# Kernel optimization log

Measured on AMD Instinct MI355X. Metric: run time of the kernel, lower is better.

Reference implementation:

```python
import jax, jax.numpy as jnp
import numpy as np

S, B, D, H = 1024, 8, 768, 12
PROMPT_NUM = 8
DH = D // H


def setup_inputs() -> dict:
    key = jax.random.key(0)
    ks = jax.random.split(key, 5)
    scale = 1.0 / np.sqrt(D)
    return {
        "x": jax.random.normal(ks[0], (S, B, D), dtype=jnp.float32),
        "in_proj_weight": jax.random.normal(ks[1], (3 * D, D), dtype=jnp.float32) * scale,
        "in_proj_bias": jax.random.normal(ks[2], (3 * D,), dtype=jnp.float32) * 0.02,
        "out_w": jax.random.normal(ks[3], (D, D), dtype=jnp.float32) * scale,
        "out_b": jax.random.normal(ks[4], (D,), dtype=jnp.float32) * 0.02,
    }


def reference(x, in_proj_weight, in_proj_bias, out_w, out_b):
    # x: (S, B, D) -> (B, S, D)
    xt = jnp.transpose(x, (1, 0, 2))
    qkv = xt @ in_proj_weight.T + in_proj_bias  # (B, S, 3D)
    q, k, v = jnp.split(qkv, 3, axis=-1)
    q = q.reshape(B, S, H, DH)
    k = k.reshape(B, S, H, DH)
    v = v.reshape(B, S, H, DH)
    # affinity (n, q, k, h); scale by sqrt(head_dim)
    aff = jnp.einsum("nqhc,nkhc->nqkh", q / np.sqrt(DH), k)
    # prompt masking: CLS_MASK | PROMPT_MASK
    tokens = S - PROMPT_NUM
    m = np.zeros((S, S), dtype=bool)
    m[0, tokens:] = True          # CLS_MASK: CLS query can't attend to prompts
    m[tokens:, tokens:] = True    # PROMPT_MASK: prompts can't attend to prompts
    m = jnp.asarray(m)
    aff = jnp.where(m[None, :, :, None], jnp.float32(-10000.0), aff)
    # softmax over key axis (dim=-2 of nqkh)
    aff = jax.nn.softmax(aff, axis=2)
    mix = jnp.einsum("nqlh,nlhc->nqhc", aff, v)  # (B, S, H, DH)
    out = mix.reshape(B, S, D) @ out_w.T + out_b
    # transpose back to (S, B, ...)
    return (
        jnp.transpose(q, (1, 0, 2, 3)),
        jnp.transpose(k, (1, 0, 2, 3)),
        jnp.transpose(v, (1, 0, 2, 3)),
        jnp.transpose(out, (1, 0, 2)),
    )
```

## Files before the change

kernel.cpp:

```cpp
#include <hip/hip_runtime.h>
#include <hip/hip_bf16.h>


typedef unsigned short u16;
typedef __attribute__((ext_vector_type(8))) short short8;
typedef __attribute__((ext_vector_type(4))) short short4v;
typedef __attribute__((ext_vector_type(4))) float floatx4;
typedef __attribute__((ext_vector_type(4))) unsigned short ushort4v;
typedef __attribute__((ext_vector_type(2))) unsigned int uint2v;

#define NB 8
#define NS 1024
#define NH 12
#define ND 768
#define DHD 64
#define TOKENS 1016
#define QKV_OUT_STRIDE 6291456

#if __has_builtin(__builtin_amdgcn_exp2f)
#define EXP2(x) __builtin_amdgcn_exp2f(x)
#else
#define EXP2(x) exp2f(x)
#endif

#if defined(__HIP_DEVICE_COMPILE__)
  #if __has_builtin(__builtin_amdgcn_mfma_f32_16x16x16bf16_1k)
    #define MFMA16(a, b, c) __builtin_amdgcn_mfma_f32_16x16x16bf16_1k(a, b, c, 0, 0, 0)
  #else
    #define MFMA16(a, b, c) __builtin_amdgcn_mfma_f32_16x16x16_bf16(a, b, c, 0, 0, 0)
  #endif
  #define GLD16(g, l)                                                        \
    __builtin_amdgcn_global_load_lds(                                        \
        (const __attribute__((address_space(1))) void*)(g),                  \
        (__attribute__((address_space(3))) void*)(l), 16, 0, 0)
#else
  #define MFMA16(a, b, c) (c)
  #define GLD16(g, l) ((void)0)
#endif

__device__ __forceinline__ u16 f2bf(float f) {
  union { float f; unsigned u; } c; c.f = f;
  return (u16)((c.u + 0x7fffu + ((c.u >> 16) & 1u)) >> 16);
}

#define CVT_B0 6144
#define CVT_B1 1728
#define CVT_B2 576
__global__ __launch_bounds__(256) void cvt3(
    const float* __restrict__ s0, u16* __restrict__ d0,
    const float* __restrict__ s1, u16* __restrict__ d1,
    const float* __restrict__ s2, u16* __restrict__ d2) {
  int blk = blockIdx.x;
  if (blk < CVT_B0) {
    const int i = (blk * 256 + (int)threadIdx.x) * 4;
    const float4 v = *(const float4*)(s0 + i);
    const int sb = i / ND;
    const int dd = i - sb * ND;
    const int m = ((sb & 7) << 10) | (sb >> 3);
    ushort4v o;
    o.x = f2bf(v.x); o.y = f2bf(v.y); o.z = f2bf(v.z); o.w = f2bf(v.w);
    *(ushort4v*)(d0 + m * ND + dd) = o;
    return;
  }
  const float* s; u16* d;
  if (blk < CVT_B0 + CVT_B1) { s = s1; d = d1; blk -= CVT_B0; }
  else { s = s2; d = d2; blk -= CVT_B0 + CVT_B1; }
  const int i = (blk * 256 + (int)threadIdx.x) * 4;
  const float4 v = *(const float4*)(s + i);
  ushort4v o;
  o.x = f2bf(v.x); o.y = f2bf(v.y); o.z = f2bf(v.z); o.w = f2bf(v.w);
  *(ushort4v*)(d + i) = o;
}

#define GEMM_STAGE(buf, k0)                                                  \
  do {                                                                       \
    GLD16(ga0 + (k0), &buf##A[c0 * 16][0]);                                  \
    GLD16(ga1 + (k0), &buf##A[c0 * 16 + 16][0]);                             \
    GLD16(gb0 + (k0), &buf##B[c0 * 16][0]);                                  \
    GLD16(gb1 + (k0), &buf##B[c0 * 16 + 16][0]);                             \
  } while (0)

#define GEMM_COMPUTE(buf)                                                    \
  do {                                                                       \
    short8 af[4], bfr[4];                                                    \
    _Pragma("unroll")                                                        \
    for (int mt = 0; mt < 4; ++mt)                                           \
      af[mt] = *(const short8*)&buf##A[wm * 64 + mt * 16 + l15][quad * 8];   \
    _Pragma("unroll")                                                        \
    for (int nt = 0; nt < 4; ++nt)                                           \
      bfr[nt] = *(const short8*)&buf##B[wn * 64 + nt * 16 + l15][quad * 8];  \
    _Pragma("unroll")                                                        \
    for (int mt = 0; mt < 4; ++mt)                                           \
      _Pragma("unroll")                                                      \
      for (int nt = 0; nt < 4; ++nt)                                         \
        acc[mt][nt] = __builtin_amdgcn_mfma_f32_16x16x32_bf16(               \
            af[mt], bfr[nt], acc[mt][nt], 0, 0, 0);                          \
  } while (0)

__global__ __launch_bounds__(256) void qkv_gemm(
    const u16* __restrict__ Xb, const u16* __restrict__ Wb,
    const float* __restrict__ bias, float* __restrict__ out) {
  __shared__ __align__(16) u16 p0A[128][32];
  __shared__ __align__(16) u16 p0B[128][32];
  __shared__ __align__(16) u16 p1A[128][32];
  __shared__ __align__(16) u16 p1B[128][32];
  const int tid = threadIdx.x;
  const int lane = tid & 63, wave = tid >> 6;
  const int l15 = lane & 15, quad = lane >> 4;
  const int wm = wave & 1, wn = wave >> 1;
  const int L = (int)blockIdx.x + 64 * (int)blockIdx.y;
  const int xcd = L & 7, i = L >> 3;
  const int mblk = (xcd + 8 * (i & 7)) * 128;
  const int nblk = (i >> 3) * 128;

  floatx4 acc[4][4];
#pragma unroll
  for (int i2 = 0; i2 < 4; ++i2)
#pragma unroll
    for (int j = 0; j < 4; ++j) acc[i2][j] = (floatx4)0.f;

  const int lr = lane >> 2;
  const int lc = (lane & 3) * 8;
  const int c0 = wave * 2;
  const int r0 = c0 * 16 + lr, r1 = r0 + 16;
  const u16* ga0 = Xb + (mblk + r0) * ND + lc;
  const u16* ga1 = Xb + (mblk + r1) * ND + lc;
  const u16* gb0 = Wb + (nblk + r0) * ND + lc;
  const u16* gb1 = Wb + (nblk + r1) * ND + lc;

  GEMM_STAGE(p0, 0);
  __syncthreads();
  for (int kt = 0; kt < 24; kt += 2) {
    GEMM_STAGE(p1, (kt + 1) * 32);
    GEMM_COMPUTE(p0);
    __syncthreads();
    if (kt + 2 < 24) GEMM_STAGE(p0, (kt + 2) * 32);
    GEMM_COMPUTE(p1);
    __syncthreads();
  }

  const int seg = nblk / ND;
  const int nbase = nblk - seg * ND;
  float* outp = out + seg * QKV_OUT_STRIDE;
#pragma unroll
  for (int mt = 0; mt < 4; ++mt) {
#pragma unroll
    for (int r = 0; r < 4; ++r) {
      const int gm = mblk + wm * 64 + mt * 16 + quad * 4 + r;
      const int b = gm >> 10, s = gm & 1023;
#pragma unroll
      for (int nt = 0; nt < 4; ++nt) {
        const int gn = nblk + wn * 64 + nt * 16 + l15;
        const int nn = nbase + wn * 64 + nt * 16 + l15;
        outp[(s * NB + b) * ND + nn] = acc[mt][nt][r] + bias[gn];
      }
    }
  }
}

__global__ __launch_bounds__(256) void prep(
    const float* __restrict__ K, const float* __restrict__ V,
    u16* __restrict__ Kb, u16* __restrict__ Vt) {
  __shared__ u16 tile[DHD][40];
  const int t = threadIdx.x;
  const int bh = blockIdx.y;
  const int b = bh / NH, h = bh % NH;
  const int s0 = blockIdx.x * 32;
  const int sl = t >> 3;
  const int c0 = (t & 7) * 8;
  const int s = s0 + sl;
  if (blockIdx.z == 0) {
    const float* src = K + ((s * NB + b) * NH + h) * DHD + c0;
    const float4 v0 = *(const float4*)src;
    const float4 v1 = *(const float4*)(src + 4);
    short8 o;
    o[0] = f2bf(v0.x); o[1] = f2bf(v0.y); o[2] = f2bf(v0.z); o[3] = f2bf(v0.w);
    o[4] = f2bf(v1.x); o[5] = f2bf(v1.y); o[6] = f2bf(v1.z); o[7] = f2bf(v1.w);
    *(short8*)(Kb + ((size_t)bh * NS + s) * DHD + c0) = o;
  } else {
    const float* src = V + ((s * NB + b) * NH + h) * DHD + c0;
    const float4 v0 = *(const float4*)src;
    const float4 v1 = *(const float4*)(src + 4);
    tile[c0 + 0][sl] = f2bf(v0.x); tile[c0 + 1][sl] = f2bf(v0.y);
    tile[c0 + 2][sl] = f2bf(v0.z); tile[c0 + 3][sl] = f2bf(v0.w);
    tile[c0 + 4][sl] = f2bf(v1.x); tile[c0 + 5][sl] = f2bf(v1.y);
    tile[c0 + 6][sl] = f2bf(v1.z); tile[c0 + 7][sl] = f2bf(v1.w);
    __syncthreads();
    const int c = t >> 2;
    const int so = (t & 3) * 8;
    *(short8*)(Vt + ((size_t)bh * DHD + c) * NS + s0 + so) =
        *(const short8*)&tile[c][so];
  }
}

__global__ __launch_bounds__(256) void attn(
    const float* __restrict__ Q, const u16* __restrict__ Kb,
    const u16* __restrict__ Vt, u16* __restrict__ mix) {
  __shared__ __align__(16) u16 Kt[64][72];
  __shared__ __align__(16) u16 Vs[64][72];
  const int tid = threadIdx.x;
  const int lane = tid & 63, wave = tid >> 6;
  const int l15 = lane & 15, quad = lane >> 4;
  const int L = (int)blockIdx.x + 8 * (int)blockIdx.y;
  const int xcd = L & 7, tt = L >> 3;
  const int bh = xcd + 8 * (tt >> 3);
  const int qx = tt & 7;
  const int b = bh / NH, h = bh % NH;
  const int qb = qx * 128 + wave * 32;

  const float SC = 0.125f * 1.44269504089f;

  short8 qf[2][2];
  bool qmask[2];
#pragma unroll
  for (int j = 0; j < 2; ++j) {
    const int qj = qb + j * 16 + l15;
    qmask[j] = (qj == 0 || qj >= TOKENS);
    const float* qp = Q + ((qj * NB + b) * NH + h) * DHD + quad * 8;
#pragma unroll
    for (int e = 0; e < 8; ++e) {
      qf[j][0][e] = (short)f2bf(qp[e] * SC);
      qf[j][1][e] = (short)f2bf(qp[32 + e] * SC);
    }
  }

  floatx4 O[2][4];
#pragma unroll
  for (int j = 0; j < 2; ++j)
#pragma unroll
    for (int g = 0; g < 4; ++g) O[j][g] = (floatx4)0.f;
  floatx4 liacc[2];
  liacc[0] = (floatx4)0.f;
  liacc[1] = (floatx4)0.f;
  short4v ones4;
#pragma unroll
  for (int e = 0; e < 4; ++e) ones4[e] = (short)0x3F80;

  const u16* kg = Kb + (size_t)bh * NS * DHD;
  const u16* vg = Vt + (size_t)bh * DHD * NS;

  const int srow = tid >> 2;
  const int scol = (tid & 3) * 16;

  short8 pk0, pk1, pv0, pv1;
  {
    pk0 = *(const short8*)(kg + srow * DHD + scol);
    pk1 = *(const short8*)(kg + srow * DHD + scol + 8);
    pv0 = *(const short8*)(vg + srow * NS + scol);
    pv1 = *(const short8*)(vg + srow * NS + scol + 8);
  }

  for (int it = 0; it < 16; ++it) {
    *(short8*)&Kt[srow][scol] = pk0;
    *(short8*)&Kt[srow][scol + 8] = pk1;
    *(short8*)&Vs[srow][scol] = pv0;
    *(short8*)&Vs[srow][scol + 8] = pv1;
    __syncthreads();
    if (it < 15) {
      const int k0 = (it + 1) * 64;
      pk0 = *(const short8*)(kg + (k0 + srow) * DHD + scol);
      pk1 = *(const short8*)(kg + (k0 + srow) * DHD + scol + 8);
      pv0 = *(const short8*)(vg + srow * NS + k0 + scol);
      pv1 = *(const short8*)(vg + srow * NS + k0 + scol + 8);
    }
    const bool mrow = (it == 15) && (quad >= 2);
#pragma unroll
    for (int sub = 0; sub < 4; ++sub) {
      const short8 kf0 = *(const short8*)&Kt[sub * 16 + l15][quad * 8];
      const short8 kf1 = *(const short8*)&Kt[sub * 16 + l15][32 + quad * 8];
      short4v pb[2];
#pragma unroll
      for (int j = 0; j < 2; ++j) {
        floatx4 a = (floatx4)0.f;
        a = __builtin_amdgcn_mfma_f32_16x16x32_bf16(kf0, qf[j][0], a, 0, 0, 0);
        a = __builtin_amdgcn_mfma_f32_16x16x32_bf16(kf1, qf[j][1], a, 0, 0, 0);
        float p[4];
#pragma unroll
        for (int r = 0; r < 4; ++r) p[r] = EXP2(a[r]);
        if (sub == 3 && mrow && qmask[j]) {
#pragma unroll
          for (int r = 0; r < 4; ++r) p[r] = 0.f;
        }
        __hip_bfloat162 w0 = __float22bfloat162_rn(make_float2(p[0], p[1]));
        __hip_bfloat162 w1 = __float22bfloat162_rn(make_float2(p[2], p[3]));
        uint2v pw;
        pw.x = *(const unsigned*)&w0;
        pw.y = *(const unsigned*)&w1;
        pb[j] = __builtin_bit_cast(short4v, pw);
      }
#pragma unroll
      for (int g = 0; g < 4; ++g) {
        const short4v vf = *(const short4v*)&Vs[g * 16 + l15][sub * 16 + quad * 4];
        O[0][g] = MFMA16(vf, pb[0], O[0][g]);
        O[1][g] = MFMA16(vf, pb[1], O[1][g]);
      }
      liacc[0] = MFMA16(ones4, pb[0], liacc[0]);
      liacc[1] = MFMA16(ones4, pb[1], liacc[1]);
    }
    __syncthreads();
  }

#pragma unroll
  for (int j = 0; j < 2; ++j) {
    const float rl = 1.0f / liacc[j][0];
    const int qj = qb + j * 16 + l15;
    u16* mp = mix + ((size_t)b * NS + qj) * ND + h * DHD + quad * 4;
#pragma unroll
    for (int g = 0; g < 4; ++g) {
      ushort4v o;
#pragma unroll
      for (int r = 0; r < 4; ++r) o[r] = f2bf(O[j][g][r] * rl);
      *(ushort4v*)(mp + g * 16) = o;
    }
  }
}

__global__ __launch_bounds__(256) void out_gemm(
    const u16* __restrict__ A, const u16* __restrict__ Wb,
    const float* __restrict__ bias, float* __restrict__ out) {
  __shared__ __align__(16) u16 p0A[128][32];
  __shared__ __align__(16) u16 p0B[128][32];
  __shared__ __align__(16) u16 p1A[128][32];
  __shared__ __align__(16) u16 p1B[128][32];
  const int tid = threadIdx.x;
  const int lane = tid & 63, wave = tid >> 6;
  const int l15 = lane & 15, quad = lane >> 4;
  const int wm = wave & 1, wn = wave >> 1;
  const int L = (int)blockIdx.x + 64 * (int)blockIdx.y;
  const int xcd = L & 7, i = L >> 3;
  const int mblk = (xcd + 8 * (i & 7)) * 128;
  const int nblk = (i >> 3) * 128;

  floatx4 acc[4][4];
#pragma unroll
  for (int i2 = 0; i2 < 4; ++i2)
#pragma unroll
    for (int j = 0; j < 4; ++j) acc[i2][j] = (floatx4)0.f;

  const int lr = lane >> 2;
  const int lc = (lane & 3) * 8;
  const int c0 = wave * 2;
  const int r0 = c0 * 16 + lr, r1 = r0 + 16;
  const u16* ga0 = A + (mblk + r0) * ND + lc;
  const u16* ga1 = A + (mblk + r1) * ND + lc;
  const u16* gb0 = Wb + (nblk + r0) * ND + lc;
  const u16* gb1 = Wb + (nblk + r1) * ND + lc;

  GEMM_STAGE(p0, 0);
  __syncthreads();
  for (int kt = 0; kt < 24; kt += 2) {
    GEMM_STAGE(p1, (kt + 1) * 32);
    GEMM_COMPUTE(p0);
    __syncthreads();
    if (kt + 2 < 24) GEMM_STAGE(p0, (kt + 2) * 32);
    GEMM_COMPUTE(p1);
    __syncthreads();
  }

#pragma unroll
  for (int mt = 0; mt < 4; ++mt) {
#pragma unroll
    for (int r = 0; r < 4; ++r) {
      const int gm = mblk + wm * 64 + mt * 16 + quad * 4 + r;
      const int b = gm >> 10, s = gm & 1023;
#pragma unroll
      for (int nt = 0; nt < 4; ++nt) {
        const int gn = nblk + wn * 64 + nt * 16 + l15;
        out[(s * NB + b) * ND + gn] = acc[mt][nt][r] + bias[gn];
      }
    }
  }
}

extern "C" void kernel_launch(void* const* d_in, const int* in_sizes, int n_in,
                              void* d_out, int out_size, void* d_ws, size_t ws_size,
                              hipStream_t stream) {
  const float* X  = (const float*)d_in[0];
  const float* W  = (const float*)d_in[1];
  const float* Bi = (const float*)d_in[2];
  const float* Ow = (const float*)d_in[3];
  const float* Ob = (const float*)d_in[4];
  float* out = (float*)d_out;

  u16* Xb  = (u16*)d_ws;
  u16* Wb  = Xb  + 6291456;
  u16* Owb = Wb  + 1769472;
  u16* Vt  = Owb + 589824;
  u16* Kb  = Vt  + 6291456;
  u16* mix = Kb  + 6291456;

  cvt3<<<CVT_B0 + CVT_B1 + CVT_B2, 256, 0, stream>>>(X, Xb, W, Wb, Ow, Owb);
  qkv_gemm<<<dim3(64, 18), 256, 0, stream>>>(Xb, Wb, Bi, out);
  prep<<<dim3(32, 96, 2), 256, 0, stream>>>(out + QKV_OUT_STRIDE,
                                            out + 2 * QKV_OUT_STRIDE, Kb, Vt);
  attn<<<dim3(8, 96), 256, 0, stream>>>(out, Kb, Vt, mix);
  out_gemm<<<dim3(64, 6), 256, 0, stream>>>(mix, Owb, Ob, out + 3 * QKV_OUT_STRIDE);
}
```

Baseline: 235.6 us.

## Fuse K bf16 conversion into QKV GEMM epilogue and double attention key tile

The QKV GEMM epilogue now also writes K as bf16 in the per-head layout, so the prep kernel only handles the V transpose and no longer rereads the fp32 K. The attention kernel stages 128 keys per iteration instead of 64, which halves the number of barrier/load rounds. It also raises wave priority with s_setprio around the PV MFMA block. Costs are extra scattered 2-byte stores in the GEMM epilogue and more LDS per block, which may lower occupancy.

```diff
diff --git a/kernel.cpp b/kernel.cpp
--- a/kernel.cpp
+++ b/kernel.cpp
@@ -33,9 +33,11 @@
     __builtin_amdgcn_global_load_lds(                                        \
         (const __attribute__((address_space(1))) void*)(g),                  \
         (__attribute__((address_space(3))) void*)(l), 16, 0, 0)
+  #define SETPRIO(n) __builtin_amdgcn_s_setprio(n)
 #else
   #define MFMA16(a, b, c) (c)
   #define GLD16(g, l) ((void)0)
+  #define SETPRIO(n) ((void)0)
 #endif
 
 __device__ __forceinline__ u16 f2bf(float f) {
@@ -99,7 +101,8 @@
 
 __global__ __launch_bounds__(256) void qkv_gemm(
     const u16* __restrict__ Xb, const u16* __restrict__ Wb,
-    const float* __restrict__ bias, float* __restrict__ out) {
+    const float* __restrict__ bias, float* __restrict__ out,
+    u16* __restrict__ Kb) {
   __shared__ __align__(16) u16 p0A[128][32];
   __shared__ __align__(16) u16 p0B[128][32];
   __shared__ __align__(16) u16 p1A[128][32];
@@ -152,15 +155,19 @@
       for (int nt = 0; nt < 4; ++nt) {
         const int gn = nblk + wn * 64 + nt * 16 + l15;
         const int nn = nbase + wn * 64 + nt * 16 + l15;
-        outp[(s * NB + b) * ND + nn] = acc[mt][nt][r] + bias[gn];
+        const float val = acc[mt][nt][r] + bias[gn];
+        outp[(s * NB + b) * ND + nn] = val;
+        if (seg == 1) {
+          Kb[(((size_t)b * NH + (nn >> 6)) * NS + s) * DHD + (nn & 63)] =
+              f2bf(val);
+        }
       }
     }
   }
 }
 
 __global__ __launch_bounds__(256) void prep(
-    const float* __restrict__ K, const float* __restrict__ V,
-    u16* __restrict__ Kb, u16* __restrict__ Vt) {
+    const float* __restrict__ V, u16* __restrict__ Vt) {
   __shared__ u16 tile[DHD][40];
   const int t = threadIdx.x;
   const int bh = blockIdx.y;
@@ -169,35 +176,25 @@
   const int sl = t >> 3;
   const int c0 = (t & 7) * 8;
   const int s = s0 + sl;
-  if (blockIdx.z == 0) {
-    const float* src = K + ((s * NB + b) * NH + h) * DHD + c0;
-    const float4 v0 = *(const float4*)src;
-    const float4 v1 = *(const float4*)(src + 4);
-    short8 o;
-    o[0] = f2bf(v0.x); o[1] = f2bf(v0.y); o[2] = f2bf(v0.z); o[3] = f2bf(v0.w);
-    o[4] = f2bf(v1.x); o[5] = f2bf(v1.y); o[6] = f2bf(v1.z); o[7] = f2bf(v1.w);
-    *(short8*)(Kb + ((size_t)bh * NS + s) * DHD + c0) = o;
-  } else {
-    const float* src = V + ((s * NB + b) * NH + h) * DHD + c0;
-    const float4 v0 = *(const float4*)src;
-    const float4 v1 = *(const float4*)(src + 4);
-    tile[c0 + 0][sl] = f2bf(v0.x); tile[c0 + 1][sl] = f2bf(v0.y);
-    tile[c0 + 2][sl] = f2bf(v0.z); tile[c0 + 3][sl] = f2bf(v0.w);
-    tile[c0 + 4][sl] = f2bf(v1.x); tile[c0 + 5][sl] = f2bf(v1.y);
-    tile[c0 + 6][sl] = f2bf(v1.z); tile[c0 + 7][sl] = f2bf(v1.w);
-    __syncthreads();
-    const int c = t >> 2;
-    const int so = (t & 3) * 8;
-    *(short8*)(Vt + ((size_t)bh * DHD + c) * NS + s0 + so) =
-        *(const short8*)&tile[c][so];
-  }
+  const float* src = V + ((s * NB + b) * NH + h) * DHD + c0;
+  const float4 v0 = *(const float4*)src;
+  const float4 v1 = *(const float4*)(src + 4);
+  tile[c0 + 0][sl] = f2bf(v0.x); tile[c0 + 1][sl] = f2bf(v0.y);
+  tile[c0 + 2][sl] = f2bf(v0.z); tile[c0 + 3][sl] = f2bf(v0.w);
+  tile[c0 + 4][sl] = f2bf(v1.x); tile[c0 + 5][sl] = f2bf(v1.y);
+  tile[c0 + 6][sl] = f2bf(v1.z); tile[c0 + 7][sl] = f2bf(v1.w);
+  __syncthreads();
+  const int c = t >> 2;
+  const int so = (t & 3) * 8;
+  *(short8*)(Vt + ((size_t)bh * DHD + c) * NS + s0 + so) =
+      *(const short8*)&tile[c][so];
 }
 
 __global__ __launch_bounds__(256) void attn(
     const float* __restrict__ Q, const u16* __restrict__ Kb,
     const u16* __restrict__ Vt, u16* __restrict__ mix) {
-  __shared__ __align__(16) u16 Kt[64][72];
-  __shared__ __align__(16) u16 Vs[64][72];
+  __shared__ __align__(16) u16 Kt[128][72];
+  __shared__ __align__(16) u16 Vs[64][136];
   const int tid = threadIdx.x;
   const int lane = tid & 63, wave = tid >> 6;
   const int l15 = lane & 15, quad = lane >> 4;
@@ -239,63 +236,73 @@
   const u16* kg = Kb + (size_t)bh * NS * DHD;
   const u16* vg = Vt + (size_t)bh * DHD * NS;
 
-  const int srow = tid >> 2;
-  const int scol = (tid & 3) * 16;
-
-  short8 pk0, pk1, pv0, pv1;
-  {
-    pk0 = *(const short8*)(kg + srow * DHD + scol);
-    pk1 = *(const short8*)(kg + srow * DHD + scol + 8);
-    pv0 = *(const short8*)(vg + srow * NS + scol);
-    pv1 = *(const short8*)(vg + srow * NS + scol + 8);
-  }
-
-  for (int it = 0; it < 16; ++it) {
-    *(short8*)&Kt[srow][scol] = pk0;
-    *(short8*)&Kt[srow][scol + 8] = pk1;
-    *(short8*)&Vs[srow][scol] = pv0;
-    *(short8*)&Vs[srow][scol + 8] = pv1;
-    __syncthreads();
-    if (it < 15) {
-      const int k0 = (it + 1) * 64;
-      pk0 = *(const short8*)(kg + (k0 + srow) * DHD + scol);
-      pk1 = *(const short8*)(kg + (k0 + srow) * DHD + scol + 8);
-      pv0 = *(const short8*)(vg + srow * NS + k0 + scol);
-      pv1 = *(const short8*)(vg + srow * NS + k0 + scol + 8);
-    }
-    const bool mrow = (it == 15) && (quad >= 2);
-#pragma unroll
-    for (int sub = 0; sub < 4; ++sub) {
-      const short8 kf0 = *(const short8*)&Kt[sub * 16 + l15][quad * 8];
-      const short8 kf1 = *(const short8*)&Kt[sub * 16 + l15][32 + quad * 8];
-      short4v pb[2];
-#pragma unroll
-      for (int j = 0; j < 2; ++j) {
-        floatx4 a = (floatx4)0.f;
-        a = __builtin_amdgcn_mfma_f32_16x16x32_bf16(kf0, qf[j][0], a, 0, 0, 0);
-        a = __builtin_amdgcn_mfma_f32_16x16x32_bf16(kf1, qf[j][1], a, 0, 0, 0);
-        float p[4];
-#pragma unroll
-        for (int r = 0; r < 4; ++r) p[r] = EXP2(a[r]);
-        if (sub == 3 && mrow && qmask[j]) {
-#pragma unroll
-          for (int r = 0; r < 4; ++r) p[r] = 0.f;
+  const int krow = tid >> 1;
+  const int kcol = (tid & 1) * 32;
+  const int vrow = tid >> 2;
+  const int vcol = (tid & 3) * 32;
+
+  short8 pk[4], pv[4];
+#pragma unroll
+  for (int u = 0; u < 4; ++u) {
+    pk[u] = *(const short8*)(kg + krow * DHD + kcol + u * 8);
+    pv[u] = *(const short8*)(vg + vrow * NS + vcol + u * 8);
+  }
+
+  for (int it = 0; it < 8; ++it) {
+#pragma unroll
+    for (int u = 0; u < 4; ++u) {
+      *(short8*)&Kt[krow][kcol + u * 8] = pk[u];
+      *(short8*)&Vs[vrow][vcol + u * 8] = pv[u];
+    }
+    __syncthreads();
+    if (it < 7) {
+      const int k0 = (it + 1) * 128;
+#pragma unroll
+      for (int u = 0; u < 4; ++u) {
+        pk[u] = *(const short8*)(kg + (k0 + krow) * DHD + kcol + u * 8);
+        pv[u] = *(const short8*)(vg + vrow * NS + k0 + vcol + u * 8);
+      }
+    }
+#pragma unroll
+    for (int half = 0; half < 2; ++half) {
+      const bool mrow = (it == 7) && (half == 1) && (quad >= 2);
+#pragma unroll
+      for (int sub = 0; sub < 4; ++sub) {
+        const int kr = half * 64 + sub * 16 + l15;
+        const short8 kf0 = *(const short8*)&Kt[kr][quad * 8];
+        const short8 kf1 = *(const short8*)&Kt[kr][32 + quad * 8];
+        short4v pb[2];
+#pragma unroll
+        for (int j = 0; j < 2; ++j) {
+          floatx4 a = (floatx4)0.f;
+          a = __builtin_amdgcn_mfma_f32_16x16x32_bf16(kf0, qf[j][0], a, 0, 0, 0);
+          a = __builtin_amdgcn_mfma_f32_16x16x32_bf16(kf1, qf[j][1], a, 0, 0, 0);
+          float p[4];
+#pragma unroll
+          for (int r = 0; r < 4; ++r) p[r] = EXP2(a[r]);
+          if (sub == 3 && mrow && qmask[j]) {
+#pragma unroll
+            for (int r = 0; r < 4; ++r) p[r] = 0.f;
+          }
+          __hip_bfloat162 w0 = __float22bfloat162_rn(make_float2(p[0], p[1]));
+          __hip_bfloat162 w1 = __float22bfloat162_rn(make_float2(p[2], p[3]));
+          uint2v pw;
+          pw.x = *(const unsigned*)&w0;
+          pw.y = *(const unsigned*)&w1;
+          pb[j] = __builtin_bit_cast(short4v, pw);
         }
-        __hip_bfloat162 w0 = __float22bfloat162_rn(make_float2(p[0], p[1]));
-        __hip_bfloat162 w1 = __float22bfloat162_rn(make_float2(p[2], p[3]));
-        uint2v pw;
-        pw.x = *(const unsigned*)&w0;
-        pw.y = *(const unsigned*)&w1;
-        pb[j] = __builtin_bit_cast(short4v, pw);
+        SETPRIO(1);
+#pragma unroll
+        for (int g = 0; g < 4; ++g) {
+          const short4v vf =
+              *(const short4v*)&Vs[g * 16 + l15][half * 64 + sub * 16 + quad * 4];
+          O[0][g] = MFMA16(vf, pb[0], O[0][g]);
+          O[1][g] = MFMA16(vf, pb[1], O[1][g]);
+        }
+        liacc[0] = MFMA16(ones4, pb[0], liacc[0]);
+        liacc[1] = MFMA16(ones4, pb[1], liacc[1]);
+        SETPRIO(0);
       }
-#pragma unroll
-      for (int g = 0; g < 4; ++g) {
-        const short4v vf = *(const short4v*)&Vs[g * 16 + l15][sub * 16 + quad * 4];
-        O[0][g] = MFMA16(vf, pb[0], O[0][g]);
-        O[1][g] = MFMA16(vf, pb[1], O[1][g]);
-      }
-      liacc[0] = MFMA16(ones4, pb[0], liacc[0]);
-      liacc[1] = MFMA16(ones4, pb[1], liacc[1]);
     }
     __syncthreads();
   }
@@ -390,9 +397,8 @@
   u16* mix = Kb  + 6291456;
 
   cvt3<<<CVT_B0 + CVT_B1 + CVT_B2, 256, 0, stream>>>(X, Xb, W, Wb, Ow, Owb);
-  qkv_gemm<<<dim3(64, 18), 256, 0, stream>>>(Xb, Wb, Bi, out);
-  prep<<<dim3(32, 96, 2), 256, 0, stream>>>(out + QKV_OUT_STRIDE,
-                                            out + 2 * QKV_OUT_STRIDE, Kb, Vt);
+  qkv_gemm<<<dim3(64, 18), 256, 0, stream>>>(Xb, Wb, Bi, out, Kb);
+  prep<<<dim3(32, 96), 256, 0, stream>>>(out + 2 * QKV_OUT_STRIDE, Vt);
   attn<<<dim3(8, 96), 256, 0, stream>>>(out, Kb, Vt, mix);
   out_gemm<<<dim3(64, 6), 256, 0, stream>>>(mix, Owb, Ob, out + 3 * QKV_OUT_STRIDE);
 }
```

New measurement: 232.1 us, median of 2. Within noise of the previous version (-1.5%).
